# Kernel optimization log

Measured on AMD Instinct MI355X. Metric: run time of the kernel, lower is better.

The kernel has to match this reference:

```python
import jax, jax.numpy as jnp
import numpy as np

TAU = 1.0

def setup_inputs() -> dict:
    key = jax.random.key(0)
    k1, k2 = jax.random.split(key)
    x = jax.random.uniform(k1, (1, 8192), dtype=jnp.float32)
    weight = jax.random.uniform(k2, (8192, 8192), dtype=jnp.float32)  # uniform_(0,1) init
    t = 128
    return {"x": x, "weight": weight, "t": t}

def reference(x, weight, t):
    # x = x / max(x) * 255 ; x = floor(x / tau)
    xq = jnp.floor((x / jnp.max(x)) * 255.0 / TAU)
    # spike mask: int32(t) == int32(x[0][i]) per element, vectorized
    spikes = (xq[0].astype(jnp.int32) == jnp.int32(t)).astype(weight.dtype)  # [in_features]
    # broadcast multiply: [out_features, in_features] * [in_features]
    return weight * spikes
```

## Files before the change

### kernel.cpp

```cpp
#include <hip/hip_runtime.h>

#define N_COLS 8192
#define LOG2_COLS 13

__global__ __launch_bounds__(1024) void spike_kernel(const float* __restrict__ x,
                                                     const int* __restrict__ t_ptr,
                                                     int* __restrict__ meta) {
    __shared__ float smax[16];
    __shared__ float s_maxv;
    __shared__ int s_count;
    const int tid = threadIdx.x;

    if (tid == 0) s_count = 0;

    float vals[8];
    float m = -1e30f;
#pragma unroll
    for (int j = 0; j < 8; ++j) {
        vals[j] = x[tid + j * 1024];
        m = fmaxf(m, vals[j]);
    }
#pragma unroll
    for (int off = 32; off > 0; off >>= 1)
        m = fmaxf(m, __shfl_down(m, off, 64));
    if ((tid & 63) == 0) smax[tid >> 6] = m;
    __syncthreads();
    if (tid < 16) {
        float mm = smax[tid];
#pragma unroll
        for (int off = 8; off > 0; off >>= 1)
            mm = fmaxf(mm, __shfl_down(mm, off, 16));
        if (tid == 0) s_maxv = mm;
    }
    __syncthreads();

    const float maxv = s_maxv;
    const int t = *t_ptr;
#pragma unroll
    for (int j = 0; j < 8; ++j) {
        const int q = (int)floorf((vals[j] / maxv) * 255.0f);
        if (q == t) {
            const int slot = atomicAdd(&s_count, 1);
            meta[1 + slot] = tid + j * 1024;
        }
    }
    __syncthreads();
    if (tid == 0) meta[0] = s_count;
}

__global__ __launch_bounds__(256) void scatter_kernel(const float* __restrict__ w,
                                                      const int* __restrict__ meta,
                                                      float* __restrict__ out) {
    const int count = meta[0];
    const int* cols = meta + 1;
    const long total = (long)count << LOG2_COLS;
    const long stride = (long)gridDim.x * blockDim.x;
    for (long idx = (long)blockIdx.x * blockDim.x + threadIdx.x; idx < total;
         idx += stride) {
        const int k = (int)(idx >> LOG2_COLS);
        const int r = (int)(idx & (N_COLS - 1));
        const long off = ((long)r << LOG2_COLS) + cols[k];
        out[off] = w[off];
    }
}

extern "C" void kernel_launch(void* const* d_in, const int* in_sizes, int n_in,
                              void* d_out, int out_size, void* d_ws, size_t ws_size,
                              hipStream_t stream) {
    const float* x = (const float*)d_in[0];
    const float* w = (const float*)d_in[1];
    const int* t = (const int*)d_in[2];
    float* out = (float*)d_out;
    int* meta = (int*)d_ws;

    spike_kernel<<<1, 1024, 0, stream>>>(x, t, meta);

    hipMemsetAsync(out, 0, (size_t)out_size * sizeof(float), stream);

    scatter_kernel<<<2048, 256, 0, stream>>>(w, meta, out);
}
```

Measured before the change: 412.8 us.

## Fuse spike detection, memset and scatter into one masked-multiply kernel

Replaces the three-step pipeline (single-block spike kernel, full-output memset, scatter of spiking columns) with one kernel. Every block recomputes the global max of x and the mask for its four columns. It then writes either the masked weights or zeros over a 32-row by 1024-column tile, using float4 accesses. This removes the separate memset pass and two launch boundaries. The cost is redundant max reduction in every block and reading weight columns whenever any of the four lanes spikes.

```diff
diff --git a/kernel.cpp b/kernel.cpp
--- a/kernel.cpp
+++ b/kernel.cpp
@@ -3,64 +3,66 @@
 #define N_COLS 8192
 #define LOG2_COLS 13
 
-__global__ __launch_bounds__(1024) void spike_kernel(const float* __restrict__ x,
-                                                     const int* __restrict__ t_ptr,
-                                                     int* __restrict__ meta) {
-    __shared__ float smax[16];
-    __shared__ float s_maxv;
-    __shared__ int s_count;
+__global__ __launch_bounds__(256) void fused_spike_mask(const float* __restrict__ x,
+                                                        const float* __restrict__ w,
+                                                        const int* __restrict__ t_ptr,
+                                                        float* __restrict__ out) {
+    __shared__ float smax[4];
     const int tid = threadIdx.x;
 
-    if (tid == 0) s_count = 0;
-
-    float vals[8];
+    const float4* __restrict__ x4 = (const float4*)x;
     float m = -1e30f;
+    float4 xv[8];
 #pragma unroll
-    for (int j = 0; j < 8; ++j) {
-        vals[j] = x[tid + j * 1024];
-        m = fmaxf(m, vals[j]);
+    for (int k = 0; k < 8; ++k) {
+        xv[k] = x4[tid + (k << 8)];
+        m = fmaxf(fmaxf(fmaxf(m, xv[k].x), fmaxf(xv[k].y, xv[k].z)), xv[k].w);
     }
 #pragma unroll
     for (int off = 32; off > 0; off >>= 1)
         m = fmaxf(m, __shfl_down(m, off, 64));
     if ((tid & 63) == 0) smax[tid >> 6] = m;
     __syncthreads();
-    if (tid < 16) {
-        float mm = smax[tid];
-#pragma unroll
-        for (int off = 8; off > 0; off >>= 1)
-            mm = fmaxf(mm, __shfl_down(mm, off, 16));
-        if (tid == 0) s_maxv = mm;
-    }
-    __syncthreads();
+    const float maxv = fmaxf(fmaxf(smax[0], smax[1]), fmaxf(smax[2], smax[3]));
 
-    const float maxv = s_maxv;
     const int t = *t_ptr;
-#pragma unroll
-    for (int j = 0; j < 8; ++j) {
-        const int q = (int)floorf((vals[j] / maxv) * 255.0f);
-        if (q == t) {
-            const int slot = atomicAdd(&s_count, 1);
-            meta[1 + slot] = tid + j * 1024;
+    const int g = ((blockIdx.x & 7) << 8) + tid;
+    const int r0 = (blockIdx.x >> 3) << 5;
+
+    const float4 xc = x4[g];
+    const int q0 = (int)floorf((xc.x / maxv) * 255.0f);
+    const int q1 = (int)floorf((xc.y / maxv) * 255.0f);
+    const int q2 = (int)floorf((xc.z / maxv) * 255.0f);
+    const int q3 = (int)floorf((xc.w / maxv) * 255.0f);
+    const float m0 = (q0 == t) ? 1.0f : 0.0f;
+    const float m1 = (q1 == t) ? 1.0f : 0.0f;
+    const float m2 = (q2 == t) ? 1.0f : 0.0f;
+    const float m3 = (q3 == t) ? 1.0f : 0.0f;
+    const bool any = (q0 == t) | (q1 == t) | (q2 == t) | (q3 == t);
+
+    const float4* __restrict__ w4 = (const float4*)w;
+    float4* __restrict__ o4 = (float4*)out;
+    size_t idx4 = ((size_t)r0 << (LOG2_COLS - 2)) + (size_t)g;
+
+    if (any) {
+#pragma unroll 8
+        for (int r = 0; r < 32; ++r) {
+            const float4 wv = w4[idx4];
+            float4 ov;
+            ov.x = wv.x * m0;
+            ov.y = wv.y * m1;
+            ov.z = wv.z * m2;
+            ov.w = wv.w * m3;
+            o4[idx4] = ov;
+            idx4 += (N_COLS >> 2);
         }
-    }
-    __syncthreads();
-    if (tid == 0) meta[0] = s_count;
-}
-
-__global__ __launch_bounds__(256) void scatter_kernel(const float* __restrict__ w,
-                                                      const int* __restrict__ meta,
-                                                      float* __restrict__ out) {
-    const int count = meta[0];
-    const int* cols = meta + 1;
-    const long total = (long)count << LOG2_COLS;
-    const long stride = (long)gridDim.x * blockDim.x;
-    for (long idx = (long)blockIdx.x * blockDim.x + threadIdx.x; idx < total;
-         idx += stride) {
-        const int k = (int)(idx >> LOG2_COLS);
-        const int r = (int)(idx & (N_COLS - 1));
-        const long off = ((long)r << LOG2_COLS) + cols[k];
-        out[off] = w[off];
+    } else {
+        const float4 z = {0.0f, 0.0f, 0.0f, 0.0f};
+#pragma unroll 8
+        for (int r = 0; r < 32; ++r) {
+            o4[idx4] = z;
+            idx4 += (N_COLS >> 2);
+        }
     }
 }
 
@@ -71,11 +73,6 @@
     const float* w = (const float*)d_in[1];
     const int* t = (const int*)d_in[2];
     float* out = (float*)d_out;
-    int* meta = (int*)d_ws;
 
-    spike_kernel<<<1, 1024, 0, stream>>>(x, t, meta);
-
-    hipMemsetAsync(out, 0, (size_t)out_size * sizeof(float), stream);
-
-    scatter_kernel<<<2048, 256, 0, stream>>>(w, meta, out);
+    fused_spike_mask<<<2048, 256, 0, stream>>>(x, w, t, out);
 }
```

Measured after the change: 428.1 us. +3.7%, slower.

## Replace memset plus column scatter with fused masked streaming write

Applied to the files above, without the earlier changes.

The spike kernel now writes a dense float mask instead of a compacted column list. The separate memset and the strided scatter kernel are replaced by one kernel that writes the whole output once with vectorized non-temporal stores. It reads weight only for 4-column groups that contain a spike and writes zeros elsewhere. This removes the double write pass and the uncoalesced column gather, but adds a mask read per thread.

```diff
diff --git a/kernel.cpp b/kernel.cpp
--- a/kernel.cpp
+++ b/kernel.cpp
@@ -1,17 +1,15 @@
 #include <hip/hip_runtime.h>
 
 #define N_COLS 8192
-#define LOG2_COLS 13
 
-__global__ __launch_bounds__(1024) void spike_kernel(const float* __restrict__ x,
-                                                     const int* __restrict__ t_ptr,
-                                                     int* __restrict__ meta) {
+typedef float floatx4 __attribute__((ext_vector_type(4)));
+
+__global__ __launch_bounds__(1024) void spike_mask_kernel(const float* __restrict__ x,
+                                                          const int* __restrict__ t_ptr,
+                                                          float* __restrict__ mask) {
     __shared__ float smax[16];
     __shared__ float s_maxv;
-    __shared__ int s_count;
     const int tid = threadIdx.x;
-
-    if (tid == 0) s_count = 0;
 
     float vals[8];
     float m = -1e30f;
@@ -39,28 +37,39 @@
 #pragma unroll
     for (int j = 0; j < 8; ++j) {
         const int q = (int)floorf((vals[j] / maxv) * 255.0f);
-        if (q == t) {
-            const int slot = atomicAdd(&s_count, 1);
-            meta[1 + slot] = tid + j * 1024;
-        }
+        mask[tid + j * 1024] = (q == t) ? 1.0f : 0.0f;
     }
-    __syncthreads();
-    if (tid == 0) meta[0] = s_count;
 }
 
-__global__ __launch_bounds__(256) void scatter_kernel(const float* __restrict__ w,
-                                                      const int* __restrict__ meta,
-                                                      float* __restrict__ out) {
-    const int count = meta[0];
-    const int* cols = meta + 1;
-    const long total = (long)count << LOG2_COLS;
-    const long stride = (long)gridDim.x * blockDim.x;
-    for (long idx = (long)blockIdx.x * blockDim.x + threadIdx.x; idx < total;
-         idx += stride) {
-        const int k = (int)(idx >> LOG2_COLS);
-        const int r = (int)(idx & (N_COLS - 1));
-        const long off = ((long)r << LOG2_COLS) + cols[k];
-        out[off] = w[off];
+__global__ __launch_bounds__(256) void stream_write_kernel(const float* __restrict__ w,
+                                                           const float* __restrict__ mask,
+                                                           float* __restrict__ out) {
+    const int tid = threadIdx.x;
+    const int g = ((blockIdx.x & 7) << 8) + tid;
+    const int r0 = (blockIdx.x >> 3) << 5;
+
+    const floatx4 mv = ((const floatx4*)mask)[g];
+    const bool any = (mv.x != 0.0f) | (mv.y != 0.0f) | (mv.z != 0.0f) | (mv.w != 0.0f);
+
+    const floatx4* __restrict__ w4 = (const floatx4*)w;
+    floatx4* __restrict__ o4 = (floatx4*)out;
+    size_t idx4 = ((size_t)r0 << 11) + (size_t)g;
+
+    if (any) {
+#pragma unroll 8
+        for (int r = 0; r < 32; ++r) {
+            const floatx4 wv = w4[idx4];
+            floatx4 ov = wv * mv;
+            __builtin_nontemporal_store(ov, &o4[idx4]);
+            idx4 += (N_COLS >> 2);
+        }
+    } else {
+        const floatx4 z = {0.0f, 0.0f, 0.0f, 0.0f};
+#pragma unroll 8
+        for (int r = 0; r < 32; ++r) {
+            __builtin_nontemporal_store(z, &o4[idx4]);
+            idx4 += (N_COLS >> 2);
+        }
     }
 }
 
@@ -71,11 +80,9 @@
     const float* w = (const float*)d_in[1];
     const int* t = (const int*)d_in[2];
     float* out = (float*)d_out;
-    int* meta = (int*)d_ws;
+    float* mask = (float*)d_ws;
 
-    spike_kernel<<<1, 1024, 0, stream>>>(x, t, meta);
+    spike_mask_kernel<<<1, 1024, 0, stream>>>(x, t, mask);
 
-    hipMemsetAsync(out, 0, (size_t)out_size * sizeof(float), stream);
-
-    scatter_kernel<<<2048, 256, 0, stream>>>(w, meta, out);
+    stream_write_kernel<<<2048, 256, 0, stream>>>(w, mask, out);
 }
```

Measured after the change: 428.1 us. +3.7%, slower.
